# Kernel tuning notes

Measured on AMD Instinct MI355X. Metric: run time of the kernel, lower is better.

The kernel has to match this reference:

```python
import jax, jax.numpy as jnp
import numpy as np

N, M, D, O = 16384, 4096, 256, 256

def setup_inputs() -> dict:
    key = jax.random.key(0)
    k1, k2, k3, k4, k5, k6, k7 = jax.random.split(key, 7)
    H_fine = jax.random.normal(k1, (N, D), dtype=jnp.float32)
    H_coarse = jax.random.normal(k2, (M, D), dtype=jnp.float32)
    inter_channel_adj = jax.random.randint(k3, (N, M), 0, 2).astype(jnp.float32)
    # attention = nn.Linear(2D, 1): weight vector [2D], bias scalar
    wa = jax.random.normal(k4, (2 * D,), dtype=jnp.float32) * (1.0 / np.sqrt(2 * D))
    ba = jax.random.normal(k5, (1,), dtype=jnp.float32) * 0.01
    # transform = nn.Linear(D, O), xavier_uniform weight
    lim = np.sqrt(6.0 / (D + O)).astype(np.float32)
    Wt = jax.random.uniform(k6, (O, D), minval=-lim, maxval=lim, dtype=jnp.float32)
    bt = jax.random.normal(k7, (O,), dtype=jnp.float32) * 0.01
    return {"H_fine": H_fine, "H_coarse": H_coarse,
            "inter_channel_adj": inter_channel_adj,
            "wa": wa, "ba": ba, "Wt": Wt, "bt": bt}

def reference(H_fine, H_coarse, inter_channel_adj, wa, ba, Wt, bt):
    d = H_fine.shape[-1]
    # additive attention: score_ij = [hf_i ; hc_j] . wa + b
    # = hf_i . wa[:d] + hc_j . wa[d:] + b  (avoids [N,M,2D] concat)
    sf = H_fine @ wa[:d]            # [N]
    sc = H_coarse @ wa[d:]          # [M]
    scores = sf[:, None] + sc[None, :] + ba[0]        # [N, M]
    masked = scores * inter_channel_adj               # [N, M]
    weights = jax.nn.softmax(masked, axis=-1)         # [N, M]
    attn_out = weights @ H_coarse                     # [N, D]
    attn_out = attn_out + H_fine                      # add_self=True
    out = attn_out @ Wt.T + bt                        # [N, O]
    return jax.nn.relu(out)
```

## Files before the change

### kernel.cpp

```cpp
#include <hip/hip_runtime.h>
#include <hip/hip_bf16.h>
#include <stdint.h>

#define N_ 16384
#define M_ 4096
#define D_ 256
#define O_ 256

#define WS_T    0
#define WS_U    65536
#define WS_R    81920
#define WS_LSUM 98304
#define WS_WTP  163840
#define WS_BP   294912
#define WS_ABM  2392064

typedef float  f32x4  __attribute__((ext_vector_type(4)));
typedef short  short8 __attribute__((ext_vector_type(8)));

__device__ __forceinline__ unsigned short f2bf(float f) {
  uint32_t u = __float_as_uint(f);
  u += 0x7FFFu + ((u >> 16) & 1u);
  return (unsigned short)(u >> 16);
}
__device__ __forceinline__ uint32_t cvtpk(float a, float b) {
  __hip_bfloat162 h = __float22bfloat162_rn(float2{a, b});
  uint32_t u;
  __builtin_memcpy(&u, &h, 4);
  return u;
}

__global__ __launch_bounds__(256) void prep_kernel(
    const float* __restrict__ Hf, const float* __restrict__ Hc,
    const float* __restrict__ wa, const float* __restrict__ ba,
    const float* __restrict__ Wt, float* __restrict__ tv,
    float* __restrict__ uv, unsigned short* __restrict__ BP,
    unsigned short* __restrict__ WtP, float* __restrict__ Rv) {
  __shared__ float tile[64][65];
  __shared__ float red[4][64];
  int b = blockIdx.x;
  int t = threadIdx.x;
  if (b < 5120) {
    int wv = t >> 6, lane = t & 63;
    const float* X; const float* w; const float* bias; float* outv; int row;
    if (b < 4096) { X = Hf; w = wa;      bias = ba;      outv = tv; row = b * 4 + wv; }
    else          { X = Hc; w = wa + D_; bias = nullptr; outv = uv; row = (b - 4096) * 4 + wv; }
    const float4* x4 = (const float4*)(X + (size_t)row * D_);
    const float4* w4 = (const float4*)w;
    float4 xa = x4[lane], wa4 = w4[lane];
    float s = xa.x * wa4.x + xa.y * wa4.y + xa.z * wa4.z + xa.w * wa4.w;
#pragma unroll
    for (int off = 32; off > 0; off >>= 1) s += __shfl_xor(s, off);
    if (lane == 0) outv[row] = expf(s + (bias ? bias[0] : 0.0f));
  } else if (b < 5376) {
    int bb = b - 5120;
    int bk = bb >> 2;
    int bc = bb & 3;
    int k0 = bk * 64, col0 = bc * 64;
    int lane = t & 63, wv = t >> 6;
    int m = lane & 15, q = lane >> 4;
    float colsum = 0.0f;
#pragma unroll
    for (int i = 0; i < 16; ++i) {
      int e = t + 256 * i;
      int kk = e >> 6, cc = e & 63;
      float v = Hc[(size_t)(k0 + kk) * D_ + col0 + cc];
      tile[kk][cc] = v;
      colsum += v;
    }
    red[wv][t & 63] = colsum;
    __syncthreads();
    if (t < 64)
      atomicAdd(&Rv[col0 + t], red[0][t] + red[1][t] + red[2][t] + red[3][t]);
#pragma unroll
    for (int t8 = 0; t8 < 2; ++t8) {
      int tile_id = t8 * 4 + wv;
      int sub = tile_id >> 2, g = tile_id & 3;
      int kgg = bk * 2 + sub;
      int cgg = bc * 4 + g;
      short8 v8;
#pragma unroll
      for (int j = 0; j < 8; ++j)
        v8[j] = (short)f2bf(tile[sub * 32 + q * 8 + j][g * 16 + m]);
      *(short8*)(BP + ((size_t)(kgg * 16 + cgg) * 64 + lane) * 8) = v8;
    }
  } else {
    int tt = (b - 5376) * 256 + t;
    int lane = tt & 63, cg = (tt >> 6) & 15, kg = tt >> 10;
    int m = lane & 15, q = lane >> 4;
    const float* src = Wt + (size_t)(cg * 16 + m) * D_ + kg * 32 + q * 8;
    float4 w0 = *(const float4*)src, w1 = *(const float4*)(src + 4);
    short8 v8;
    v8[0] = (short)f2bf(w0.x); v8[1] = (short)f2bf(w0.y);
    v8[2] = (short)f2bf(w0.z); v8[3] = (short)f2bf(w0.w);
    v8[4] = (short)f2bf(w1.x); v8[5] = (short)f2bf(w1.y);
    v8[6] = (short)f2bf(w1.z); v8[7] = (short)f2bf(w1.w);
    *(short8*)(WtP + (size_t)tt * 8) = v8;
  }
}

__global__ __launch_bounds__(256) void pack_bits_kernel(
    const float* __restrict__ adj, const float* __restrict__ tv,
    const float* __restrict__ uv, unsigned long long* __restrict__ ABM,
    float* __restrict__ Lsum) {
  __shared__ float u_lds[M_];
  int tid = threadIdx.x;
  int w = tid >> 6, lane = tid & 63;
  for (int i = tid; i < M_; i += 256) u_lds[i] = uv[i];
  __syncthreads();
  int r0 = (blockIdx.x * 4 + w) * 2;
  const float* arA = adj + (size_t)r0 * M_;
  const float* arB = arA + M_;
  float suA = 0.f, scA = 0.f, suB = 0.f, scB = 0.f;

  float a0 = arA[lane], a1 = arA[64 + lane], a2 = arA[128 + lane], a3 = arA[192 + lane];
  float b0 = arB[lane], b1 = arB[64 + lane], b2 = arB[128 + lane], b3 = arB[192 + lane];
#pragma unroll 1
  for (int i = 0; i < 16; ++i) {
    int k0 = i * 256;
    int k1 = (i + 1 < 16) ? k0 + 256 : 0;
    float na0 = arA[k1 + lane],       na1 = arA[k1 + 64 + lane];
    float na2 = arA[k1 + 128 + lane], na3 = arA[k1 + 192 + lane];
    float nb0 = arB[k1 + lane],       nb1 = arB[k1 + 64 + lane];
    float nb2 = arB[k1 + 128 + lane], nb3 = arB[k1 + 192 + lane];

    unsigned long long wA0 = __ballot(a0 != 0.0f), wA1 = __ballot(a1 != 0.0f);
    unsigned long long wA2 = __ballot(a2 != 0.0f), wA3 = __ballot(a3 != 0.0f);
    unsigned long long wB0 = __ballot(b0 != 0.0f), wB1 = __ballot(b1 != 0.0f);
    unsigned long long wB2 = __ballot(b2 != 0.0f), wB3 = __ballot(b3 != 0.0f);
    suA = fmaf(a0, u_lds[k0 + lane], suA);
    suA = fmaf(a1, u_lds[k0 + 64 + lane], suA);
    suA = fmaf(a2, u_lds[k0 + 128 + lane], suA);
    suA = fmaf(a3, u_lds[k0 + 192 + lane], suA);
    scA += (a0 + a1) + (a2 + a3);
    suB = fmaf(b0, u_lds[k0 + lane], suB);
    suB = fmaf(b1, u_lds[k0 + 64 + lane], suB);
    suB = fmaf(b2, u_lds[k0 + 128 + lane], suB);
    suB = fmaf(b3, u_lds[k0 + 192 + lane], suB);
    scB += (b0 + b1) + (b2 + b3);
    if (lane < 8) {
      int sel = lane & 3;
      unsigned long long vA = sel == 0 ? wA0 : sel == 1 ? wA1 : sel == 2 ? wA2 : wA3;
      unsigned long long vB = sel == 0 ? wB0 : sel == 1 ? wB1 : sel == 2 ? wB2 : wB3;
      int r = (lane < 4) ? r0 : r0 + 1;
      ABM[(size_t)r * 64 + i * 4 + sel] = (lane < 4) ? vA : vB;
    }
    a0 = na0; a1 = na1; a2 = na2; a3 = na3;
    b0 = nb0; b1 = nb1; b2 = nb2; b3 = nb3;
  }
#pragma unroll
  for (int off = 32; off > 0; off >>= 1) {
    suA += __shfl_xor(suA, off); scA += __shfl_xor(scA, off);
    suB += __shfl_xor(suB, off); scB += __shfl_xor(scB, off);
  }
  if (lane == 0) {
    Lsum[r0] = tv[r0] * suA - scA;
    Lsum[r0 + 1] = tv[r0 + 1] * suB - scB;
  }
}

__device__ __forceinline__ short8 frag_bits(uint32_t bits, float t,
                                            float4 u0, float4 u1) {
  float c[8];
  c[0] = fmaf(t, u0.x, -1.0f); c[1] = fmaf(t, u0.y, -1.0f);
  c[2] = fmaf(t, u0.z, -1.0f); c[3] = fmaf(t, u0.w, -1.0f);
  c[4] = fmaf(t, u1.x, -1.0f); c[5] = fmaf(t, u1.y, -1.0f);
  c[6] = fmaf(t, u1.z, -1.0f); c[7] = fmaf(t, u1.w, -1.0f);
  union { short8 s; uint32_t u[4]; } r;
#pragma unroll
  for (int p = 0; p < 4; ++p) {
    uint32_t mlo = 0u - ((bits >> (2 * p)) & 1u);
    uint32_t mhi = 0u - ((bits >> (2 * p + 1)) & 1u);
    r.u[p] = cvtpk(c[2 * p], c[2 * p + 1]) &
             ((mlo & 0x0000FFFFu) | (mhi & 0xFFFF0000u));
  }
  return r.s;
}

__global__ __launch_bounds__(1024, 4) void mega_kernel(
    const unsigned int* __restrict__ ABM32, const unsigned short* __restrict__ BP,
    const float* __restrict__ tv, const float* __restrict__ uv,
    const float* __restrict__ Lsum, const float* __restrict__ Rv,
    const float* __restrict__ Hf, const unsigned short* __restrict__ WtP,
    const float* __restrict__ bt, float* __restrict__ out) {
  __shared__ __align__(16) char smem[114944];
  unsigned int (*bt2)[129] = (unsigned int (*)[129])(smem);
  float* u_lds = (float*)(smem + 33024);
  float (*Cred)[256] = (float (*)[256])(smem + 49408);
  unsigned short (*attn)[264] = (unsigned short (*)[264])(smem);

  int tid = threadIdx.x;
  int w = tid >> 6, lane = tid & 63;
  int q = lane >> 4, m = lane & 15;
  int colq = w >> 2, ksub = w & 3;
  int i0 = blockIdx.x * 64;

  const unsigned short* bbase = BP + (size_t)(colq * 4) * 512 + (size_t)lane * 8;
  int kg0 = ksub * 32;
  short8 curB[4];
#pragma unroll
  for (int n = 0; n < 4; ++n)
    curB[n] = *(const short8*)(bbase + ((size_t)kg0 * 16 + n) * 512);
  float t0 = tv[i0 + m], t1 = tv[i0 + 16 + m];
  float t2 = tv[i0 + 32 + m], t3 = tv[i0 + 48 + m];

  for (int i = tid; i < M_; i += 1024) u_lds[i] = uv[i];
  for (int p = tid; p < 8192; p += 1024) {
    int row = p >> 7, word = p & 127;
    bt2[row][word] = ABM32[(size_t)(i0 + row) * 128 + word];
  }

  f32x4 acc[4][4];
#pragma unroll
  for (int s = 0; s < 4; ++s)
#pragma unroll
    for (int n = 0; n < 4; ++n) acc[s][n] = (f32x4){0.f, 0.f, 0.f, 0.f};

  __syncthreads();

  for (int it = 0; it < 32; ++it) {
    int kg = kg0 + it;
    int kn = (it + 1 < 32) ? kg + 1 : kg0;
    short8 nB[4];
#pragma unroll
    for (int n = 0; n < 4; ++n)
      nB[n] = *(const short8*)(bbase + ((size_t)kn * 16 + n) * 512);

    float4 u0 = *(const float4*)&u_lds[kg * 32 + q * 8];
    float4 u1 = *(const float4*)&u_lds[kg * 32 + q * 8 + 4];
    uint32_t b0 = bt2[m][kg],      b1 = bt2[16 + m][kg];
    uint32_t b2 = bt2[32 + m][kg], b3 = bt2[48 + m][kg];
    int sh = q * 8;
    short8 af0 = frag_bits((b0 >> sh) & 0xffu, t0, u0, u1);
    short8 af1 = frag_bits((b1 >> sh) & 0xffu, t1, u0, u1);
    short8 af2 = frag_bits((b2 >> sh) & 0xffu, t2, u0, u1);
    short8 af3 = frag_bits((b3 >> sh) & 0xffu, t3, u0, u1);
#pragma unroll
    for (int n = 0; n < 4; ++n) {
      acc[0][n] = __builtin_amdgcn_mfma_f32_16x16x32_bf16(af0, curB[n], acc[0][n], 0, 0, 0);
      acc[1][n] = __builtin_amdgcn_mfma_f32_16x16x32_bf16(af1, curB[n], acc[1][n], 0, 0, 0);
      acc[2][n] = __builtin_amdgcn_mfma_f32_16x16x32_bf16(af2, curB[n], acc[2][n], 0, 0, 0);
      acc[3][n] = __builtin_amdgcn_mfma_f32_16x16x32_bf16(af3, curB[n], acc[3][n], 0, 0, 0);
    }
#pragma unroll
    for (int n = 0; n < 4; ++n) curB[n] = nB[n];
  }

#pragma unroll
  for (int s4 = 0; s4 < 4; ++s4) {
    if (ksub == s4) {
#pragma unroll
      for (int s = 0; s < 4; ++s)
#pragma unroll
        for (int n = 0; n < 4; ++n) {
          int col = colq * 64 + n * 16 + m;
#pragma unroll
          for (int r = 0; r < 4; ++r) {
            int rl = s * 16 + q * 4 + r;
            if (s4 == 0) Cred[rl][col] = acc[s][n][r];
            else         Cred[rl][col] += acc[s][n][r];
          }
        }
    }
    __syncthreads();
  }

  {
    int row = tid >> 4;
    int c0 = (tid & 15) * 16;
    size_t grow = (size_t)i0 + row;
    float invL = 1.0f / (Lsum[grow] + (float)M_);
    const float* hfp = Hf + grow * D_ + c0;
    const float* rvp = Rv + c0;
    const float* crp = &Cred[row][c0];
#pragma unroll
    for (int g = 0; g < 4; ++g) {
      float4 cv = *(const float4*)(crp + g * 4);
      float4 rv = *(const float4*)(rvp + g * 4);
      float4 hv = *(const float4*)(hfp + g * 4);
      float v0 = fmaf(cv.x + rv.x, invL, hv.x);
      float v1 = fmaf(cv.y + rv.y, invL, hv.y);
      float v2 = fmaf(cv.z + rv.z, invL, hv.z);
      float v3 = fmaf(cv.w + rv.w, invL, hv.w);
      *(uint32_t*)&attn[row][c0 + g * 4]     = cvtpk(v0, v1);
      *(uint32_t*)&attn[row][c0 + g * 4 + 2] = cvtpk(v2, v3);
    }
  }
  __syncthreads();

  {
    int rt = w & 3, cq = w >> 2;
    f32x4 facc[4];
#pragma unroll
    for (int n = 0; n < 4; ++n) facc[n] = (f32x4){0.f, 0.f, 0.f, 0.f};
    const unsigned short* wwave = WtP + (size_t)(cq * 4) * 512 + (size_t)lane * 8;
#pragma unroll
    for (int kf = 0; kf < 8; ++kf) {
      short8 af = *(const short8*)&attn[rt * 16 + m][kf * 32 + q * 8];
#pragma unroll
      for (int n = 0; n < 4; ++n) {
        short8 bf = *(const short8*)(wwave + ((size_t)kf * 16 + n) * 512);
        facc[n] = __builtin_amdgcn_mfma_f32_16x16x32_bf16(af, bf, facc[n], 0, 0, 0);
      }
    }
#pragma unroll
    for (int n = 0; n < 4; ++n) {
      int col = cq * 64 + n * 16 + m;
      float b = bt[col];
#pragma unroll
      for (int r = 0; r < 4; ++r) {
        size_t row = (size_t)i0 + rt * 16 + q * 4 + r;
        out[row * O_ + col] = fmaxf(facc[n][r] + b, 0.0f);
      }
    }
  }
}

extern "C" void kernel_launch(void* const* d_in, const int* in_sizes, int n_in,
                              void* d_out, int out_size, void* d_ws, size_t ws_size,
                              hipStream_t stream) {
  const float* Hf  = (const float*)d_in[0];
  const float* Hc  = (const float*)d_in[1];
  const float* adj = (const float*)d_in[2];
  const float* wa  = (const float*)d_in[3];
  const float* ba  = (const float*)d_in[4];
  const float* Wt  = (const float*)d_in[5];
  const float* bt  = (const float*)d_in[6];
  float* out = (float*)d_out;

  char* ws = (char*)d_ws;
  float* tv   = (float*)(ws + WS_T);
  float* uv   = (float*)(ws + WS_U);
  float* Rv   = (float*)(ws + WS_R);
  float* Lsum = (float*)(ws + WS_LSUM);
  unsigned short* WtP = (unsigned short*)(ws + WS_WTP);
  unsigned short* BP  = (unsigned short*)(ws + WS_BP);
  unsigned long long* ABM = (unsigned long long*)(ws + WS_ABM);

  hipMemsetAsync(Rv, 0, D_ * sizeof(float), stream);

  prep_kernel<<<5408, 256, 0, stream>>>(Hf, Hc, wa, ba, Wt, tv, uv, BP, WtP, Rv);
  pack_bits_kernel<<<2048, 256, 0, stream>>>(adj, tv, uv, ABM, Lsum);
  mega_kernel<<<256, 1024, 0, stream>>>((const unsigned int*)ABM, BP, tv, uv,
                                        Lsum, Rv, Hf, WtP, bt, out);
}
```

Baseline: 470.6 us.

## Fuse adjacency bit-packing and row-sum pass into main attention kernel

```diff
diff --git a/kernel.cpp b/kernel.cpp
--- a/kernel.cpp
+++ b/kernel.cpp
@@ -10,10 +10,8 @@
 #define WS_T    0
 #define WS_U    65536
 #define WS_R    81920
-#define WS_LSUM 98304
-#define WS_WTP  163840
-#define WS_BP   294912
-#define WS_ABM  2392064
+#define WS_WTP  98304
+#define WS_BP   229376
 
 typedef float  f32x4  __attribute__((ext_vector_type(4)));
 typedef short  short8 __attribute__((ext_vector_type(8)));
@@ -99,66 +97,6 @@
   }
 }
 
-__global__ __launch_bounds__(256) void pack_bits_kernel(
-    const float* __restrict__ adj, const float* __restrict__ tv,
-    const float* __restrict__ uv, unsigned long long* __restrict__ ABM,
-    float* __restrict__ Lsum) {
-  __shared__ float u_lds[M_];
-  int tid = threadIdx.x;
-  int w = tid >> 6, lane = tid & 63;
-  for (int i = tid; i < M_; i += 256) u_lds[i] = uv[i];
-  __syncthreads();
-  int r0 = (blockIdx.x * 4 + w) * 2;
-  const float* arA = adj + (size_t)r0 * M_;
-  const float* arB = arA + M_;
-  float suA = 0.f, scA = 0.f, suB = 0.f, scB = 0.f;
-
-  float a0 = arA[lane], a1 = arA[64 + lane], a2 = arA[128 + lane], a3 = arA[192 + lane];
-  float b0 = arB[lane], b1 = arB[64 + lane], b2 = arB[128 + lane], b3 = arB[192 + lane];
-#pragma unroll 1
-  for (int i = 0; i < 16; ++i) {
-    int k0 = i * 256;
-    int k1 = (i + 1 < 16) ? k0 + 256 : 0;
-    float na0 = arA[k1 + lane],       na1 = arA[k1 + 64 + lane];
-    float na2 = arA[k1 + 128 + lane], na3 = arA[k1 + 192 + lane];
-    float nb0 = arB[k1 + lane],       nb1 = arB[k1 + 64 + lane];
-    float nb2 = arB[k1 + 128 + lane], nb3 = arB[k1 + 192 + lane];
-
-    unsigned long long wA0 = __ballot(a0 != 0.0f), wA1 = __ballot(a1 != 0.0f);
-    unsigned long long wA2 = __ballot(a2 != 0.0f), wA3 = __ballot(a3 != 0.0f);
-    unsigned long long wB0 = __ballot(b0 != 0.0f), wB1 = __ballot(b1 != 0.0f);
-    unsigned long long wB2 = __ballot(b2 != 0.0f), wB3 = __ballot(b3 != 0.0f);
-    suA = fmaf(a0, u_lds[k0 + lane], suA);
-    suA = fmaf(a1, u_lds[k0 + 64 + lane], suA);
-    suA = fmaf(a2, u_lds[k0 + 128 + lane], suA);
-    suA = fmaf(a3, u_lds[k0 + 192 + lane], suA);
-    scA += (a0 + a1) + (a2 + a3);
-    suB = fmaf(b0, u_lds[k0 + lane], suB);
-    suB = fmaf(b1, u_lds[k0 + 64 + lane], suB);
-    suB = fmaf(b2, u_lds[k0 + 128 + lane], suB);
-    suB = fmaf(b3, u_lds[k0 + 192 + lane], suB);
-    scB += (b0 + b1) + (b2 + b3);
-    if (lane < 8) {
-      int sel = lane & 3;
-      unsigned long long vA = sel == 0 ? wA0 : sel == 1 ? wA1 : sel == 2 ? wA2 : wA3;
-      unsigned long long vB = sel == 0 ? wB0 : sel == 1 ? wB1 : sel == 2 ? wB2 : wB3;
-      int r = (lane < 4) ? r0 : r0 + 1;
-      ABM[(size_t)r * 64 + i * 4 + sel] = (lane < 4) ? vA : vB;
-    }
-    a0 = na0; a1 = na1; a2 = na2; a3 = na3;
-    b0 = nb0; b1 = nb1; b2 = nb2; b3 = nb3;
-  }
-#pragma unroll
-  for (int off = 32; off > 0; off >>= 1) {
-    suA += __shfl_xor(suA, off); scA += __shfl_xor(scA, off);
-    suB += __shfl_xor(suB, off); scB += __shfl_xor(scB, off);
-  }
-  if (lane == 0) {
-    Lsum[r0] = tv[r0] * suA - scA;
-    Lsum[r0 + 1] = tv[r0 + 1] * suB - scB;
-  }
-}
-
 __device__ __forceinline__ short8 frag_bits(uint32_t bits, float t,
                                             float4 u0, float4 u1) {
   float c[8];
@@ -169,8 +107,8 @@
   union { short8 s; uint32_t u[4]; } r;
 #pragma unroll
   for (int p = 0; p < 4; ++p) {
-    uint32_t mlo = 0u - ((bits >> (2 * p)) & 1u);
-    uint32_t mhi = 0u - ((bits >> (2 * p + 1)) & 1u);
+    uint32_t mlo = (uint32_t)((int32_t)(bits << (31 - 2 * p)) >> 31);
+    uint32_t mhi = (uint32_t)((int32_t)(bits << (30 - 2 * p)) >> 31);
     r.u[p] = cvtpk(c[2 * p], c[2 * p + 1]) &
              ((mlo & 0x0000FFFFu) | (mhi & 0xFFFF0000u));
   }
@@ -178,15 +116,16 @@
 }
 
 __global__ __launch_bounds__(1024, 4) void mega_kernel(
-    const unsigned int* __restrict__ ABM32, const unsigned short* __restrict__ BP,
+    const float* __restrict__ adj, const unsigned short* __restrict__ BP,
     const float* __restrict__ tv, const float* __restrict__ uv,
-    const float* __restrict__ Lsum, const float* __restrict__ Rv,
-    const float* __restrict__ Hf, const unsigned short* __restrict__ WtP,
-    const float* __restrict__ bt, float* __restrict__ out) {
-  __shared__ __align__(16) char smem[114944];
+    const float* __restrict__ Rv, const float* __restrict__ Hf,
+    const unsigned short* __restrict__ WtP, const float* __restrict__ bt,
+    float* __restrict__ out) {
+  __shared__ __align__(16) char smem[115200];
   unsigned int (*bt2)[129] = (unsigned int (*)[129])(smem);
   float* u_lds = (float*)(smem + 33024);
   float (*Cred)[256] = (float (*)[256])(smem + 49408);
+  float* Lsum_lds = (float*)(smem + 114944);
   unsigned short (*attn)[264] = (unsigned short (*)[264])(smem);
 
   int tid = threadIdx.x;
@@ -195,6 +134,62 @@
   int colq = w >> 2, ksub = w & 3;
   int i0 = blockIdx.x * 64;
 
+  for (int i = tid; i < M_; i += 1024) u_lds[i] = uv[i];
+  __syncthreads();
+
+#pragma unroll 1
+  for (int pass = 0; pass < 2; ++pass) {
+    int r0 = w * 4 + pass * 2;
+    const float* arA = adj + ((size_t)i0 + r0) * M_;
+    const float* arB = arA + M_;
+    float suA = 0.f, scA = 0.f, suB = 0.f, scB = 0.f;
+    float a0 = arA[lane], a1 = arA[64 + lane], a2 = arA[128 + lane], a3 = arA[192 + lane];
+    float b0 = arB[lane], b1 = arB[64 + lane], b2 = arB[128 + lane], b3 = arB[192 + lane];
+#pragma unroll 1
+    for (int i = 0; i < 16; ++i) {
+      int k0 = i * 256;
+      int k1 = (i + 1 < 16) ? k0 + 256 : 0;
+      float na0 = arA[k1 + lane],       na1 = arA[k1 + 64 + lane];
+      float na2 = arA[k1 + 128 + lane], na3 = arA[k1 + 192 + lane];
+      float nb0 = arB[k1 + lane],       nb1 = arB[k1 + 64 + lane];
+      float nb2 = arB[k1 + 128 + lane], nb3 = arB[k1 + 192 + lane];
+
+      unsigned long long wA0 = __ballot(a0 != 0.0f), wA1 = __ballot(a1 != 0.0f);
+      unsigned long long wA2 = __ballot(a2 != 0.0f), wA3 = __ballot(a3 != 0.0f);
+      unsigned long long wB0 = __ballot(b0 != 0.0f), wB1 = __ballot(b1 != 0.0f);
+      unsigned long long wB2 = __ballot(b2 != 0.0f), wB3 = __ballot(b3 != 0.0f);
+      suA = fmaf(a0, u_lds[k0 + lane], suA);
+      suA = fmaf(a1, u_lds[k0 + 64 + lane], suA);
+      suA = fmaf(a2, u_lds[k0 + 128 + lane], suA);
+      suA = fmaf(a3, u_lds[k0 + 192 + lane], suA);
+      scA += (a0 + a1) + (a2 + a3);
+      suB = fmaf(b0, u_lds[k0 + lane], suB);
+      suB = fmaf(b1, u_lds[k0 + 64 + lane], suB);
+      suB = fmaf(b2, u_lds[k0 + 128 + lane], suB);
+      suB = fmaf(b3, u_lds[k0 + 192 + lane], suB);
+      scB += (b0 + b1) + (b2 + b3);
+      if (lane < 16) {
+        int rowsel = lane >> 3;
+        int c = (lane >> 1) & 3, hi = lane & 1;
+        unsigned long long v = rowsel ? (c == 0 ? wB0 : c == 1 ? wB1 : c == 2 ? wB2 : wB3)
+                                      : (c == 0 ? wA0 : c == 1 ? wA1 : c == 2 ? wA2 : wA3);
+        bt2[r0 + rowsel][i * 8 + c * 2 + hi] =
+            hi ? (unsigned int)(v >> 32) : (unsigned int)v;
+      }
+      a0 = na0; a1 = na1; a2 = na2; a3 = na3;
+      b0 = nb0; b1 = nb1; b2 = nb2; b3 = nb3;
+    }
+#pragma unroll
+    for (int off = 32; off > 0; off >>= 1) {
+      suA += __shfl_xor(suA, off); scA += __shfl_xor(scA, off);
+      suB += __shfl_xor(suB, off); scB += __shfl_xor(scB, off);
+    }
+    if (lane == 0) {
+      Lsum_lds[r0]     = tv[i0 + r0] * suA - scA;
+      Lsum_lds[r0 + 1] = tv[i0 + r0 + 1] * suB - scB;
+    }
+  }
+
   const unsigned short* bbase = BP + (size_t)(colq * 4) * 512 + (size_t)lane * 8;
   int kg0 = ksub * 32;
   short8 curB[4];
@@ -203,12 +198,6 @@
     curB[n] = *(const short8*)(bbase + ((size_t)kg0 * 16 + n) * 512);
   float t0 = tv[i0 + m], t1 = tv[i0 + 16 + m];
   float t2 = tv[i0 + 32 + m], t3 = tv[i0 + 48 + m];
-
-  for (int i = tid; i < M_; i += 1024) u_lds[i] = uv[i];
-  for (int p = tid; p < 8192; p += 1024) {
-    int row = p >> 7, word = p & 127;
-    bt2[row][word] = ABM32[(size_t)(i0 + row) * 128 + word];
-  }
 
   f32x4 acc[4][4];
 #pragma unroll
@@ -269,7 +258,7 @@
     int row = tid >> 4;
     int c0 = (tid & 15) * 16;
     size_t grow = (size_t)i0 + row;
-    float invL = 1.0f / (Lsum[grow] + (float)M_);
+    float invL = 1.0f / (Lsum_lds[row] + (float)M_);
     const float* hfp = Hf + grow * D_ + c0;
     const float* rvp = Rv + c0;
     const float* crp = &Cred[row][c0];
@@ -332,15 +321,11 @@
   float* tv   = (float*)(ws + WS_T);
   float* uv   = (float*)(ws + WS_U);
   float* Rv   = (float*)(ws + WS_R);
-  float* Lsum = (float*)(ws + WS_LSUM);
   unsigned short* WtP = (unsigned short*)(ws + WS_WTP);
   unsigned short* BP  = (unsigned short*)(ws + WS_BP);
-  unsigned long long* ABM = (unsigned long long*)(ws + WS_ABM);
 
   hipMemsetAsync(Rv, 0, D_ * sizeof(float), stream);
 
   prep_kernel<<<5408, 256, 0, stream>>>(Hf, Hc, wa, ba, Wt, tv, uv, BP, WtP, Rv);
-  pack_bits_kernel<<<2048, 256, 0, stream>>>(adj, tv, uv, ABM, Lsum);
-  mega_kernel<<<256, 1024, 0, stream>>>((const unsigned int*)ABM, BP, tv, uv,
-                                        Lsum, Rv, Hf, WtP, bt, out);
-}
+  mega_kernel<<<256, 1024, 0, stream>>>(adj, BP, tv, uv, Rv, Hf, WtP, bt, out);
+}
```

Measured after the change: 462.4 us. No clear change (-1.7%).
